# Kernel optimization log

Hardware: AMD Instinct MI355X
Metric: run time of the kernel (lower is better)

Reference implementation:

```python
import jax, jax.numpy as jnp
import numpy as np

NEG_SLOPE = 0.2
CONV3_NUM, CONV1_NUM, POLY_NUM = 3, 5, 4
FEAT_DIM = CONV3_NUM * 84 + CONV1_NUM * 12 + POLY_NUM * 12  # 360
DN = ('NCHW', 'OIHW', 'NCHW')


def leaky_relu(x):
    return jnp.where(x >= 0, x, NEG_SLOPE * x)


def conv3x3(x, feat):
    # per-sample dynamic 3x3 conv: feat[:, :81] -> kernel [3,3,3,3], feat[:, 81:84] -> bias
    B = x.shape[0]
    k = feat[:, :81].reshape(B, 3, 3, 3, 3)
    b = feat[:, 81:84]

    def one(xi, ki, bi):
        y = jax.lax.conv_general_dilated(xi[None], ki, (1, 1), 'SAME', dimension_numbers=DN)[0]
        return y + bi[:, None, None]

    return leaky_relu(jax.vmap(one)(x, k, b))


def conv1x1(x, feat):
    B = x.shape[0]
    k = feat[:, :9].reshape(B, 3, 3, 1, 1)
    b = feat[:, 9:12]

    def one(xi, ki, bi):
        y = jax.lax.conv_general_dilated(xi[None], ki, (1, 1), 'VALID', dimension_numbers=DN)[0]
        return y + bi[:, None, None]

    return leaky_relu(jax.vmap(one)(x, k, b))


def conv_stack(x, feature):
    residual = x
    for i in range(CONV3_NUM):
        x = conv3x3(x, feature[:, i * 84:(i + 1) * 84])
    off = CONV3_NUM * 84
    for i in range(CONV1_NUM):
        x = conv1x1(x, feature[:, off + i * 12:off + (i + 1) * 12])
    return residual + x


def att_map(feat, h_mat, w_mat, xc):
    # product over POLY_NUM of (a*h + b*w + c*x + d)
    att = jnp.ones_like(xc)
    for i in range(POLY_NUM):
        a = feat[:, i * 4 + 0].reshape(-1, 1, 1, 1)
        b = feat[:, i * 4 + 1].reshape(-1, 1, 1, 1)
        c = feat[:, i * 4 + 2].reshape(-1, 1, 1, 1)
        d = feat[:, i * 4 + 3].reshape(-1, 1, 1, 1)
        att = att * (a * h_mat + b * w_mat + c * xc + d)
    return att


def apply_attention(x, feature):
    H, W = x.shape[2], x.shape[3]
    h_mat = (jnp.arange(H, dtype=x.dtype) / H).reshape(1, 1, H, 1)
    w_mat = (jnp.arange(W, dtype=x.dtype) / W).reshape(1, 1, 1, W)
    off = CONV3_NUM * 84 + CONV1_NUM * 12
    atts = [att_map(feature[:, off + c * POLY_NUM * 4: off + (c + 1) * POLY_NUM * 4],
                    h_mat, w_mat, x[:, c:c + 1]) for c in range(3)]  # R, G, B
    att = jnp.concatenate(atts, axis=1)
    return x * (1 + att)


def setup_inputs() -> dict:
    key = jax.random.key(0)
    k1, k2, k3 = jax.random.split(key, 3)
    x = jax.random.uniform(k1, (8, 3, 512, 512), dtype=jnp.float32)
    thumb_x = jax.random.uniform(k2, (8, 3, 64, 64), dtype=jnp.float32)
    Wm = jax.random.normal(k3, (3, FEAT_DIM), dtype=jnp.float32) * 0.05
    bm = jnp.zeros((FEAT_DIM,), dtype=jnp.float32)
    return {"x": x, "thumb_x": thumb_x, "Wm": Wm, "bm": bm}


def reference(x, thumb_x, Wm, bm):
    # meta: GAP over thumbnail -> linear -> per-sample hypernetwork features [B, 360]
    feature = jnp.mean(thumb_x, axis=(2, 3)) @ Wm + bm
    x = conv_stack(x, feature)
    x = apply_attention(x, feature)
    thumb = conv_stack(thumb_x, feature)
    thumb = apply_attention(thumb, feature)
    return (x, thumb)
```

## Files before the change

### kernel.cpp

```cpp
#include <hip/hip_runtime.h>


typedef float v2f __attribute__((ext_vector_type(2)));
#define FMA2(a, b, c) __builtin_elementwise_fma((a), (b), (c))

__device__ __forceinline__ v2f leaky2(v2f v) {
    return __builtin_elementwise_max(v, v * 0.2f);
}

__device__ __forceinline__ v2f ldpair(const float* p) {
    v2f r; __builtin_memcpy(&r, p, 8); return r;
}
__device__ __forceinline__ void stpair(float* p, v2f v) {
    __builtin_memcpy(p, &v, 8);
}

constexpr int NCOLS = 73;
constexpr int CSTRA = 23;
constexpr int CHSA  = NCOLS * CSTRA;
constexpr int ASZ   = 3 * CHSA + 4;
constexpr int CSTRB = 21;
constexpr int CHSB  = NCOLS * CSTRB;
constexpr int BSZ   = 3 * CHSB + 4;

__global__ __launch_bounds__(384) void prep_kernel(
    const float* __restrict__ thumb, const float* __restrict__ Wm,
    const float* __restrict__ bm, float* __restrict__ feat)
{
    const int b = blockIdx.x;
    const int t = threadIdx.x;
    const int ch = t >> 7;
    const int l  = t & 127;
    const float4* p = (const float4*)(thumb + (size_t)b * 3 * 4096);
    float s = 0.f;
#pragma unroll
    for (int k = 0; k < 8; ++k) {
        float4 v = p[ch * 1024 + l + k * 128];
        s += v.x + v.y + v.z + v.w;
    }
    __shared__ float red[384];
    red[t] = s;
    __syncthreads();
    for (int off = 64; off > 0; off >>= 1) {
        if (l < off) red[t] += red[t + off];
        __syncthreads();
    }
    if (t < 360) {
        const float sc = 1.f / 4096.f;
        const float m0 = red[0] * sc, m1 = red[128] * sc, m2 = red[256] * sc;
        feat[b * 360 + t] =
            fmaf(m0, Wm[t], fmaf(m1, Wm[360 + t], fmaf(m2, Wm[720 + t], bm[t])));
    }
}

template<int CHS_, int CSTR_, int NC>
__device__ __forceinline__ void conv_rows_pk(
    const float* __restrict__ buf, const float* __restrict__ fw,
    int rb, int gx, v2f acc[3][NC])
{
    const float b0 = fw[81], b1 = fw[82], b2 = fw[83];
#pragma unroll
    for (int c = 0; c < NC; ++c) {
        v2f i0 = {b0, b0}; v2f i1 = {b1, b1}; v2f i2 = {b2, b2};
        acc[0][c] = i0; acc[1][c] = i1; acc[2][c] = i2;
    }
    const int c0 = (gx < 0) ? 3 : gx + 3;
#pragma unroll
    for (int ich = 0; ich < 3; ++ich) {
        const int base = ich * CHS_ + rb;
        v2f p0[NC + 2], p1[NC + 2], pm[NC + 2];
#pragma unroll
        for (int k = 0; k < NC + 2; ++k) {
            const int cc = (k == 0) ? c0 : (gx + 3 + k);
            p0[k] = ldpair(&buf[base + cc * CSTR_]);
            p1[k] = ldpair(&buf[base + cc * CSTR_ + 2]);
            v2f m = {p0[k].y, p1[k].x};
            pm[k] = m;
        }
#pragma unroll
        for (int dy = 0; dy < 3; ++dy) {
#pragma unroll
            for (int oc = 0; oc < 3; ++oc) {
                const float w0 = fw[oc * 27 + ich * 9 + dy * 3 + 0];
                const float w1 = fw[oc * 27 + ich * 9 + dy * 3 + 1];
                const float w2 = fw[oc * 27 + ich * 9 + dy * 3 + 2];
                v2f W0 = {w0, w0}; v2f W1 = {w1, w1}; v2f W2 = {w2, w2};
#pragma unroll
                for (int c = 0; c < NC; ++c) {
                    const v2f wa = (dy == 0) ? p0[c]     : (dy == 1) ? pm[c]     : p1[c];
                    const v2f wb = (dy == 0) ? p0[c + 1] : (dy == 1) ? pm[c + 1] : p1[c + 1];
                    const v2f wc = (dy == 0) ? p0[c + 2] : (dy == 1) ? pm[c + 2] : p1[c + 2];
                    acc[oc][c] = FMA2(wa, W0, FMA2(wb, W1, FMA2(wc, W2, acc[oc][c])));
                }
            }
        }
    }
}

__global__ __launch_bounds__(256, 4) void conv_att_kernel(
    const float* __restrict__ x, const float* __restrict__ thumb,
    const float* __restrict__ feat, float* __restrict__ out)
{
    __shared__ float bufA[ASZ];
    __shared__ float bufB[BSZ];

    int id = blockIdx.x;
    const float* src; float* dst; int H, W, b, trow, tcol;
    if (id < 2048) {
        b = id >> 8; const int t = id & 255;
        H = 512; W = 512; trow = (t >> 3) * 16; tcol = (t & 7) * 64;
        src = x; dst = out;
    } else {
        const int i2 = id - 2048;
        b = i2 >> 2; trow = (i2 & 3) * 16; tcol = 0;
        H = 64; W = 64; src = thumb;
        dst = out + (size_t)8 * 3 * 512 * 512;
    }
    const float* fb = feat + b * 360;
    const int tid = threadIdx.x;

    const float* sbg = src + (size_t)b * 3 * H * W;
    float4 stv[4];
#pragma unroll
    for (int i = 0; i < 4; ++i) {
        const int q = tid + 256 * i;
        const int c = q / 352;
        const int rem = q - c * 352;
        const int mr = rem >> 4;
        const int k  = rem & 15;
        const int gr = trow + mr - 3;
        const int gc0 = tcol + 4 * k;
        float4 v = make_float4(0.f, 0.f, 0.f, 0.f);
        if ((unsigned)gr < (unsigned)H)
            v = *(const float4*)&sbg[(size_t)c * H * W + (size_t)gr * W + gc0];
        stv[i] = v;
    }
    const bool has5 = tid < 32;
    float4 st5 = make_float4(0.f, 0.f, 0.f, 0.f);
    if (has5) {
        const int q = tid + 1024;
        const int rem = q - 704;
        const int mr = rem >> 4;
        const int k  = rem & 15;
        const int gr = trow + mr - 3;
        const int gc0 = tcol + 4 * k;
        if ((unsigned)gr < (unsigned)H)
            st5 = *(const float4*)&sbg[(size_t)2 * H * W + (size_t)gr * W + gc0];
    }
    const bool hasH = tid < 132;
    float4 hv = make_float4(0.f, 0.f, 0.f, 0.f);
    int hc = 0, hmr = 0, hside = 0;
    if (hasH) {
        hc = tid / 44;
        const int rem = tid - hc * 44;
        hmr = rem >> 1;
        hside = rem & 1;
        const int gr = trow + hmr - 3;
        const int gc0 = tcol + (hside ? 64 : -4);
        const bool rok = (unsigned)gr < (unsigned)H;
        const float* gp = sbg + (size_t)hc * H * W + (size_t)(rok ? gr : 0) * W;
        if (rok && (unsigned)gc0 <= (unsigned)(W - 4)) {
            hv = *(const float4*)&gp[gc0];
        } else {
            hv.x = (rok && (unsigned)(gc0 + 0) < (unsigned)W) ? gp[gc0 + 0] : 0.f;
            hv.y = (rok && (unsigned)(gc0 + 1) < (unsigned)W) ? gp[gc0 + 1] : 0.f;
            hv.z = (rok && (unsigned)(gc0 + 2) < (unsigned)W) ? gp[gc0 + 2] : 0.f;
            hv.w = (rok && (unsigned)(gc0 + 3) < (unsigned)W) ? gp[gc0 + 3] : 0.f;
        }
    }
#pragma unroll
    for (int i = 0; i < 4; ++i) {
        const int q = tid + 256 * i;
        const int c = q / 352;
        const int rem = q - c * 352;
        const int mr = rem >> 4;
        const int k  = rem & 15;
        float* bp = &bufA[c * CHSA + (4 * k + 4) * CSTRA + mr];
        bp[0] = stv[i].x; bp[CSTRA] = stv[i].y;
        bp[2 * CSTRA] = stv[i].z; bp[3 * CSTRA] = stv[i].w;
    }
    if (has5) {
        const int rem = tid + 1024 - 704;
        const int mr = rem >> 4;
        const int k  = rem & 15;
        float* bp = &bufA[2 * CHSA + (4 * k + 4) * CSTRA + mr];
        bp[0] = st5.x; bp[CSTRA] = st5.y; bp[2 * CSTRA] = st5.z; bp[3 * CSTRA] = st5.w;
    }
    if (hasH) {
        float* bp = &bufA[hc * CHSA + (hside ? 68 : 0) * CSTRA + hmr];
        bp[0] = hv.x; bp[CSTRA] = hv.y; bp[2 * CSTRA] = hv.z; bp[3 * CSTRA] = hv.w;
    }
    if (tid < 66) {
        const int c = tid / 22, mr = tid - c * 22;
        bufA[c * CHSA + 72 * CSTRA + mr] = 0.f;
    } else if (tid < 126) {
        const int t2 = tid - 66;
        const int c = t2 / 20, r = t2 - c * 20;
        bufB[c * CHSB + 72 * CSTRB + r] = 0.f;
    }
    __syncthreads();

    const int s3e = tid >> 5;
    const int gx3e = 2 * (tid & 31);
    v2f res2[3][2];
#pragma unroll
    for (int ch = 0; ch < 3; ++ch)
#pragma unroll
        for (int c = 0; c < 2; ++c)
            res2[ch][c] = ldpair(&bufA[ch * CHSA + (gx3e + 4 + c) * CSTRA + (2 * s3e + 3)]);
    {
        const bool act1 = tid < 180;
        int s1, gx1;
        if (tid < 160) { s1 = tid >> 4; gx1 = 4 * (tid & 15); }
        else { const int v = tid - 160; s1 = v >> 1; gx1 = (v & 1) ? 64 : -4; }
        if (act1) {
            v2f acc[3][4];
            conv_rows_pk<CHSA, CSTRA, 4>(bufA, fb, 2 * s1, gx1, acc);
#pragma unroll
            for (int oc = 0; oc < 3; ++oc)
#pragma unroll
                for (int c = 0; c < 4; ++c)
                    stpair(&bufB[oc * CHSB + (gx1 + 4 + c) * CSTRB + 2 * s1],
                           leaky2(acc[oc][c]));
        }
    }
    __syncthreads();

    {
        const bool act2 = tid < 162;
        int s2, gx2;
        if (tid < 144) { s2 = tid >> 4; gx2 = 4 * (tid & 15); }
        else { const int v = tid - 144; s2 = v >> 1; gx2 = (v & 1) ? 64 : -4; }
        if (act2) {
            v2f acc[3][4];
            conv_rows_pk<CHSB, CSTRB, 4>(bufB, fb + 84, 2 * s2, gx2, acc);
#pragma unroll
            for (int oc = 0; oc < 3; ++oc)
#pragma unroll
                for (int c = 0; c < 4; ++c)
                    stpair(&bufA[oc * CHSA + (gx2 + 4 + c) * CSTRA + 2 * s2 + 2],
                           leaky2(acc[oc][c]));
        }
    }
    __syncthreads();

    {
        v2f y[3][2];
        {
            v2f acc3[3][2];
            conv_rows_pk<CHSA, CSTRA, 2>(bufA, fb + 168, 2 * s3e + 2, gx3e, acc3);
#pragma unroll
            for (int oc = 0; oc < 3; ++oc)
#pragma unroll
                for (int c = 0; c < 2; ++c) y[oc][c] = leaky2(acc3[oc][c]);
        }

#pragma unroll
        for (int lay = 0; lay < 5; ++lay) {
            const float* fw = fb + 252 + lay * 12;
            v2f W0 = {fw[0], fw[0]}; v2f W1 = {fw[1], fw[1]}; v2f W2 = {fw[2], fw[2]};
            v2f W3 = {fw[3], fw[3]}; v2f W4 = {fw[4], fw[4]}; v2f W5 = {fw[5], fw[5]};
            v2f W6 = {fw[6], fw[6]}; v2f W7 = {fw[7], fw[7]}; v2f W8 = {fw[8], fw[8]};
            v2f C0 = {fw[9], fw[9]}; v2f C1 = {fw[10], fw[10]}; v2f C2 = {fw[11], fw[11]};
            v2f z0[2], z1[2], z2[2];
#pragma unroll
            for (int c = 0; c < 2; ++c) {
                z0[c] = FMA2(y[0][c], W0, FMA2(y[1][c], W1, FMA2(y[2][c], W2, C0)));
                z1[c] = FMA2(y[0][c], W3, FMA2(y[1][c], W4, FMA2(y[2][c], W5, C1)));
                z2[c] = FMA2(y[0][c], W6, FMA2(y[1][c], W7, FMA2(y[2][c], W8, C2)));
            }
#pragma unroll
            for (int c = 0; c < 2; ++c) {
                y[0][c] = leaky2(z0[c]);
                y[1][c] = leaky2(z1[c]);
                y[2][c] = leaky2(z2[c]);
            }
        }

        const float invH = 1.f / (float)H;
        const float invW = 1.f / (float)W;
        const int gr0 = trow + 2 * s3e;
        v2f h2 = {(float)gr0 * invH, (float)(gr0 + 1) * invH};
        const float wb = (float)(tcol + gx3e) * invW;
        const v2f one = {1.f, 1.f};
#pragma unroll
        for (int ch = 0; ch < 3; ++ch) {
            const float* fp = fb + 312 + ch * 16;
            v2f PA0 = {fp[0], fp[0]},  PB0 = {fp[1], fp[1]},  PC0 = {fp[2], fp[2]},  PD0 = {fp[3], fp[3]};
            v2f PA1 = {fp[4], fp[4]},  PB1 = {fp[5], fp[5]},  PC1 = {fp[6], fp[6]},  PD1 = {fp[7], fp[7]};
            v2f PA2 = {fp[8], fp[8]},  PB2 = {fp[9], fp[9]},  PC2 = {fp[10], fp[10]}, PD2 = {fp[11], fp[11]};
            v2f PA3 = {fp[12], fp[12]}, PB3 = {fp[13], fp[13]}, PC3 = {fp[14], fp[14]}, PD3 = {fp[15], fp[15]};
            v2f t0 = FMA2(PA0, h2, PD0);
            v2f t1 = FMA2(PA1, h2, PD1);
            v2f t2 = FMA2(PA2, h2, PD2);
            v2f t3 = FMA2(PA3, h2, PD3);
            v2f o[2];
#pragma unroll
            for (int c = 0; c < 2; ++c) {
                const float wcs = wb + (float)c * invW;
                v2f Wc = {wcs, wcs};
                v2f v = y[ch][c] + res2[ch][c];
                v2f a = FMA2(PB0, Wc, FMA2(PC0, v, t0));
                a = a * FMA2(PB1, Wc, FMA2(PC1, v, t1));
                a = a * FMA2(PB2, Wc, FMA2(PC2, v, t2));
                a = a * FMA2(PB3, Wc, FMA2(PC3, v, t3));
                o[c] = v * (one + a);
            }
            v2f ra = {o[0].x, o[1].x};
            v2f rb2 = {o[0].y, o[1].y};
            float* dp = &dst[((size_t)(b * 3 + ch) * H + gr0) * W + tcol + gx3e];
            __builtin_memcpy(dp, &ra, 8);
            __builtin_memcpy(dp + W, &rb2, 8);
        }
    }
}

extern "C" void kernel_launch(void* const* d_in, const int* in_sizes, int n_in,
                              void* d_out, int out_size, void* d_ws, size_t ws_size,
                              hipStream_t stream) {
    const float* x = (const float*)d_in[0];
    const float* thumb = (const float*)d_in[1];
    const float* Wm = (const float*)d_in[2];
    const float* bm = (const float*)d_in[3];
    float* out = (float*)d_out;
    float* feat = (float*)d_ws;

    prep_kernel<<<8, 384, 0, stream>>>(thumb, Wm, bm, feat);
    conv_att_kernel<<<2080, 256, 0, stream>>>(x, thumb, feat, out);
}
```

Measured before the change: 106.5 us.

## Double tile height and use single in-place shared buffer with 512 threads

Tiles grow from 16 to 32 output rows with 512-thread blocks, which reduces the relative halo recomputation overhead of the three fused 3x3 convs. The two ping-pong shared buffers are merged into one buffer updated in place. Each conv's results are held in registers across an extra barrier before being written back. This adds barriers and more shared memory per block, which may reduce occupancy, in exchange for less redundant halo loading and compute.

Result: slower. 113.0 us (+6.1%).

```diff
diff --git a/kernel.cpp b/kernel.cpp
--- a/kernel.cpp
+++ b/kernel.cpp
@@ -16,12 +16,10 @@
 }
 
 constexpr int NCOLS = 73;
-constexpr int CSTRA = 23;
-constexpr int CHSA  = NCOLS * CSTRA;
-constexpr int ASZ   = 3 * CHSA + 4;
-constexpr int CSTRB = 21;
-constexpr int CHSB  = NCOLS * CSTRB;
-constexpr int BSZ   = 3 * CHSB + 4;
+constexpr int ROWS0 = 38;
+constexpr int CSTR  = 39;
+constexpr int CHS   = NCOLS * CSTR;
+constexpr int BUFSZ = 3 * CHS + 4;
 
 __global__ __launch_bounds__(384) void prep_kernel(
     const float* __restrict__ thumb, const float* __restrict__ Wm,
@@ -53,7 +51,7 @@
     }
 }
 
-template<int CHS_, int CSTR_, int NC>
+template<int NC>
 __device__ __forceinline__ void conv_rows_pk(
     const float* __restrict__ buf, const float* __restrict__ fw,
     int rb, int gx, v2f acc[3][NC])
@@ -67,13 +65,13 @@
     const int c0 = (gx < 0) ? 3 : gx + 3;
 #pragma unroll
     for (int ich = 0; ich < 3; ++ich) {
-        const int base = ich * CHS_ + rb;
+        const int base = ich * CHS + rb;
         v2f p0[NC + 2], p1[NC + 2], pm[NC + 2];
 #pragma unroll
         for (int k = 0; k < NC + 2; ++k) {
             const int cc = (k == 0) ? c0 : (gx + 3 + k);
-            p0[k] = ldpair(&buf[base + cc * CSTR_]);
-            p1[k] = ldpair(&buf[base + cc * CSTR_ + 2]);
+            p0[k] = ldpair(&buf[base + cc * CSTR]);
+            p1[k] = ldpair(&buf[base + cc * CSTR + 2]);
             v2f m = {p0[k].y, p1[k].x};
             pm[k] = m;
         }
@@ -97,22 +95,21 @@
     }
 }
 
-__global__ __launch_bounds__(256, 4) void conv_att_kernel(
+__global__ __launch_bounds__(512, 4) void conv_att_kernel(
     const float* __restrict__ x, const float* __restrict__ thumb,
     const float* __restrict__ feat, float* __restrict__ out)
 {
-    __shared__ float bufA[ASZ];
-    __shared__ float bufB[BSZ];
+    __shared__ float buf[BUFSZ];
 
     int id = blockIdx.x;
     const float* src; float* dst; int H, W, b, trow, tcol;
-    if (id < 2048) {
-        b = id >> 8; const int t = id & 255;
-        H = 512; W = 512; trow = (t >> 3) * 16; tcol = (t & 7) * 64;
+    if (id < 1024) {
+        b = id >> 7; const int t = id & 127;
+        H = 512; W = 512; trow = (t >> 3) * 32; tcol = (t & 7) * 64;
         src = x; dst = out;
     } else {
-        const int i2 = id - 2048;
-        b = i2 >> 2; trow = (i2 & 3) * 16; tcol = 0;
+        const int i2 = id - 1024;
+        b = i2 >> 1; trow = (i2 & 1) * 32; tcol = 0;
         H = 64; W = 64; src = thumb;
         dst = out + (size_t)8 * 3 * 512 * 512;
     }
@@ -120,12 +117,12 @@
     const int tid = threadIdx.x;
 
     const float* sbg = src + (size_t)b * 3 * H * W;
-    float4 stv[4];
-#pragma unroll
-    for (int i = 0; i < 4; ++i) {
-        const int q = tid + 256 * i;
-        const int c = q / 352;
-        const int rem = q - c * 352;
+    float4 stv[3];
+#pragma unroll
+    for (int i = 0; i < 3; ++i) {
+        const int q = tid + 512 * i;
+        const int c = q / 608;
+        const int rem = q - c * 608;
         const int mr = rem >> 4;
         const int k  = rem & 15;
         const int gr = trow + mr - 3;
@@ -135,24 +132,23 @@
             v = *(const float4*)&sbg[(size_t)c * H * W + (size_t)gr * W + gc0];
         stv[i] = v;
     }
-    const bool has5 = tid < 32;
-    float4 st5 = make_float4(0.f, 0.f, 0.f, 0.f);
-    if (has5) {
-        const int q = tid + 1024;
-        const int rem = q - 704;
+    const bool has4 = tid < 288;
+    float4 st4 = make_float4(0.f, 0.f, 0.f, 0.f);
+    if (has4) {
+        const int rem = tid + 1536 - 1216;
         const int mr = rem >> 4;
         const int k  = rem & 15;
         const int gr = trow + mr - 3;
         const int gc0 = tcol + 4 * k;
         if ((unsigned)gr < (unsigned)H)
-            st5 = *(const float4*)&sbg[(size_t)2 * H * W + (size_t)gr * W + gc0];
-    }
-    const bool hasH = tid < 132;
+            st4 = *(const float4*)&sbg[(size_t)2 * H * W + (size_t)gr * W + gc0];
+    }
+    const bool hasH = tid < 228;
     float4 hv = make_float4(0.f, 0.f, 0.f, 0.f);
     int hc = 0, hmr = 0, hside = 0;
     if (hasH) {
-        hc = tid / 44;
-        const int rem = tid - hc * 44;
+        hc = tid / 76;
+        const int rem = tid - hc * 76;
         hmr = rem >> 1;
         hside = rem & 1;
         const int gr = trow + hmr - 3;
@@ -169,36 +165,39 @@
         }
     }
 #pragma unroll
-    for (int i = 0; i < 4; ++i) {
-        const int q = tid + 256 * i;
-        const int c = q / 352;
-        const int rem = q - c * 352;
+    for (int i = 0; i < 3; ++i) {
+        const int q = tid + 512 * i;
+        const int c = q / 608;
+        const int rem = q - c * 608;
         const int mr = rem >> 4;
         const int k  = rem & 15;
-        float* bp = &bufA[c * CHSA + (4 * k + 4) * CSTRA + mr];
-        bp[0] = stv[i].x; bp[CSTRA] = stv[i].y;
-        bp[2 * CSTRA] = stv[i].z; bp[3 * CSTRA] = stv[i].w;
-    }
-    if (has5) {
-        const int rem = tid + 1024 - 704;
+        float* bp = &buf[c * CHS + (4 * k + 4) * CSTR + mr];
+        bp[0] = stv[i].x; bp[CSTR] = stv[i].y;
+        bp[2 * CSTR] = stv[i].z; bp[3 * CSTR] = stv[i].w;
+    }
+    if (has4) {
+        const int rem = tid + 1536 - 1216;
         const int mr = rem >> 4;
         const int k  = rem & 15;
-        float* bp = &bufA[2 * CHSA + (4 * k + 4) * CSTRA + mr];
-        bp[0] = st5.x; bp[CSTRA] = st5.y; bp[2 * CSTRA] = st5.z; bp[3 * CSTRA] = st5.w;
+        float* bp = &buf[2 * CHS + (4 * k + 4) * CSTR + mr];
+        bp[0] = st4.x; bp[CSTR] = st4.y; bp[2 * CSTR] = st4.z; bp[3 * CSTR] = st4.w;
     }
     if (hasH) {
-        float* bp = &bufA[hc * CHSA + (hside ? 68 : 0) * CSTRA + hmr];
-        bp[0] = hv.x; bp[CSTRA] = hv.y; bp[2 * CSTRA] = hv.z; bp[3 * CSTRA] = hv.w;
-    }
-    if (tid < 66) {
-        const int c = tid / 22, mr = tid - c * 22;
-        bufA[c * CHSA + 72 * CSTRA + mr] = 0.f;
-    } else if (tid < 126) {
-        const int t2 = tid - 66;
-        const int c = t2 / 20, r = t2 - c * 20;
-        bufB[c * CHSB + 72 * CSTRB + r] = 0.f;
-    }
-    __syncthreads();
+        float* bp = &buf[hc * CHS + (hside ? 68 : 0) * CSTR + hmr];
+        bp[0] = hv.x; bp[CSTR] = hv.y; bp[2 * CSTR] = hv.z; bp[3 * CSTR] = hv.w;
+    }
+    if (tid < 114) {
+        const int c = tid / 38, r = tid - c * 38;
+        buf[c * CHS + 72 * CSTR + r] = 0.f;
+    }
+    __syncthreads();
+
+    const bool act1 = tid < 324;
+    int s1, gx1;
+    if (tid < 288) { s1 = tid >> 4; gx1 = 4 * (tid & 15); }
+    else { const int v = tid - 288; s1 = v >> 1; gx1 = (v & 1) ? 64 : -4; }
+    v2f acc[3][4];
+    if (act1) conv_rows_pk<4>(buf, fb, 2 * s1, gx1, acc);
 
     const int s3e = tid >> 5;
     const int gx3e = 2 * (tid & 31);
@@ -207,40 +206,33 @@
     for (int ch = 0; ch < 3; ++ch)
 #pragma unroll
         for (int c = 0; c < 2; ++c)
-            res2[ch][c] = ldpair(&bufA[ch * CHSA + (gx3e + 4 + c) * CSTRA + (2 * s3e + 3)]);
-    {
-        const bool act1 = tid < 180;
-        int s1, gx1;
-        if (tid < 160) { s1 = tid >> 4; gx1 = 4 * (tid & 15); }
-        else { const int v = tid - 160; s1 = v >> 1; gx1 = (v & 1) ? 64 : -4; }
-        if (act1) {
-            v2f acc[3][4];
-            conv_rows_pk<CHSA, CSTRA, 4>(bufA, fb, 2 * s1, gx1, acc);
-#pragma unroll
-            for (int oc = 0; oc < 3; ++oc)
-#pragma unroll
-                for (int c = 0; c < 4; ++c)
-                    stpair(&bufB[oc * CHSB + (gx1 + 4 + c) * CSTRB + 2 * s1],
-                           leaky2(acc[oc][c]));
-        }
-    }
-    __syncthreads();
-
-    {
-        const bool act2 = tid < 162;
-        int s2, gx2;
-        if (tid < 144) { s2 = tid >> 4; gx2 = 4 * (tid & 15); }
-        else { const int v = tid - 144; s2 = v >> 1; gx2 = (v & 1) ? 64 : -4; }
-        if (act2) {
-            v2f acc[3][4];
-            conv_rows_pk<CHSB, CSTRB, 4>(bufB, fb + 84, 2 * s2, gx2, acc);
-#pragma unroll
-            for (int oc = 0; oc < 3; ++oc)
-#pragma unroll
-                for (int c = 0; c < 4; ++c)
-                    stpair(&bufA[oc * CHSA + (gx2 + 4 + c) * CSTRA + 2 * s2 + 2],
-                           leaky2(acc[oc][c]));
-        }
+            res2[ch][c] = ldpair(&buf[ch * CHS + (gx3e + 4 + c) * CSTR + (2 * s3e + 3)]);
+    __syncthreads();
+
+    if (act1) {
+#pragma unroll
+        for (int oc = 0; oc < 3; ++oc)
+#pragma unroll
+            for (int c = 0; c < 4; ++c)
+                stpair(&buf[oc * CHS + (gx1 + 4 + c) * CSTR + (2 * s1 + 1)],
+                       leaky2(acc[oc][c]));
+    }
+    __syncthreads();
+
+    const bool act2 = tid < 306;
+    int s2, gx2;
+    if (tid < 272) { s2 = tid >> 4; gx2 = 4 * (tid & 15); }
+    else { const int v = tid - 272; s2 = v >> 1; gx2 = (v & 1) ? 64 : -4; }
+    if (act2) conv_rows_pk<4>(buf, fb + 84, 2 * s2 + 1, gx2, acc);
+    __syncthreads();
+
+    if (act2) {
+#pragma unroll
+        for (int oc = 0; oc < 3; ++oc)
+#pragma unroll
+            for (int c = 0; c < 4; ++c)
+                stpair(&buf[oc * CHS + (gx2 + 4 + c) * CSTR + (2 * s2 + 2)],
+                       leaky2(acc[oc][c]));
     }
     __syncthreads();
 
@@ -248,7 +240,7 @@
         v2f y[3][2];
         {
             v2f acc3[3][2];
-            conv_rows_pk<CHSA, CSTRA, 2>(bufA, fb + 168, 2 * s3e + 2, gx3e, acc3);
+            conv_rows_pk<2>(buf, fb + 168, 2 * s3e + 2, gx3e, acc3);
 #pragma unroll
             for (int oc = 0; oc < 3; ++oc)
 #pragma unroll
@@ -326,5 +318,5 @@
     float* feat = (float*)d_ws;
 
     prep_kernel<<<8, 384, 0, stream>>>(thumb, Wm, bm, feat);
-    conv_att_kernel<<<2080, 256, 0, stream>>>(x, thumb, feat, out);
-}
+    conv_att_kernel<<<1040, 512, 0, stream>>>(x, thumb, feat, out);
+}
```
